# Kernel optimization log

Hardware: AMD Instinct MI355X
Metric: run time of the kernel (lower is better)

Reference implementation:

```python
import jax, jax.numpy as jnp
import numpy as np

F = 16      # frames
NV = 4096   # visual points per frame
NT = 512    # tactile points per frame
M = 4096    # model points
SCALE = 0.1


def setup_inputs() -> dict:
    key = jax.random.key(0)
    ks = jax.random.split(key, 6)
    return {
        "state": jax.random.normal(ks[0], (6,), dtype=jnp.float32) * 0.1,
        "model_points": jax.random.normal(ks[1], (M, 3), dtype=jnp.float32),
        "visual_points": jax.random.normal(ks[2], (F, NV, 3), dtype=jnp.float32),
        "tactile_points": jax.random.normal(ks[3], (F, NT, 3), dtype=jnp.float32),
        "physics_pred_states": jax.random.normal(ks[4], (F, 12), dtype=jnp.float32) * 0.1,
        "delta_time": jax.random.uniform(ks[5], (F,), dtype=jnp.float32, minval=0.01, maxval=0.05),
    }


def _skew(a):
    z = jnp.zeros((), a.dtype)
    return jnp.array([[z, -a[2], a[1]],
                      [a[2], z, -a[0]],
                      [-a[1], a[0], z]])


def _rot_from_omega(omega, dt):
    # Rodrigues: R = I + sin(theta*dt) S + (1 - cos(theta*dt)) S@S, S = skew(omega/|omega|)
    theta = jnp.linalg.norm(omega)
    ax = omega / jnp.clip(theta, 1e-8)
    S = _skew(ax)
    return jnp.eye(3, dtype=omega.dtype) + jnp.sin(theta * dt) * S + (1.0 - jnp.cos(theta * dt)) * (S @ S)


def _chamfer(pred, gt):
    # rows: pred [N,3], cols: gt [M,3]; row-min of squared distances, then mean
    d = (jnp.sum(pred * pred, axis=1)[:, None]
         + jnp.sum(gt * gt, axis=1)[None, :]
         - 2.0 * pred @ gt.T)
    return jnp.mean(jnp.min(d, axis=1))


def reference(state, model_points, visual_points, tactile_points, physics_pred_states, delta_time):
    t0 = state[:3]
    r0 = _rot_from_omega(state[3:], jnp.float32(1.0))  # Euler2Mat modeled as axis-angle

    def pose_step(carry, x):
        t, r = carry
        v, omega, dt = x
        t = t + v * dt
        r = _rot_from_omega(omega, dt) @ r
        return (t, r), (t, r)

    _, (ts, rs) = jax.lax.scan(
        pose_step, (t0, r0),
        (physics_pred_states[1:, 6:9], physics_pred_states[1:, 9:12], delta_time[1:]))
    ts = jnp.concatenate([t0[None], ts], axis=0)  # [F,3]
    rs = jnp.concatenate([r0[None], rs], axis=0)  # [F,3,3]

    def frame_loss(acc, x):
        t, r, vp, tp = x
        vc = ((vp - t) @ r) / SCALE
        tc = ((tp - t) @ r) / SCALE
        acc = acc + _chamfer(vc, model_points) + 0.1 * _chamfer(tc, model_points)
        return acc, None

    E_cd, _ = jax.lax.scan(frame_loss, jnp.zeros((), jnp.float32),
                           (ts, rs, visual_points, tactile_points))
    return E_cd
```

## Files before the change

### kernel.cpp

```cpp
#include <hip/hip_runtime.h>
#include <math.h>

#define F_    16
#define NV_   4096
#define NT_   512
#define M_    4096
#define PPF_  (NV_ + NT_)
#define NPTS_ (F_ * PPF_)
#define SCALE_INV 10.0f

#define TPB   256
#define PTSB  96
#define NBLK  (NPTS_ / PTSB)
#define NG    32
#define MPG   (M_ / NG)
#define CHM   32
#define NCH   (MPG / CHM)
#define FS    33
#define PPL   12
#define NPR   6

typedef float v2f __attribute__((ext_vector_type(2)));
typedef float v4f __attribute__((ext_vector_type(4)));

__device__ inline void rot_from_omega(float ox, float oy, float oz, float dt,
                                      float* R) {
    float theta = sqrtf(ox * ox + oy * oy + oz * oz);
    float inv = 1.0f / fmaxf(theta, 1e-8f);
    float ax = ox * inv, ay = oy * inv, az = oz * inv;
    float s = sinf(theta * dt);
    float c = 1.0f - cosf(theta * dt);
    R[0] = 1.0f - c * (ay * ay + az * az);
    R[1] = -s * az + c * ax * ay;
    R[2] =  s * ay + c * ax * az;
    R[3] =  s * az + c * ax * ay;
    R[4] = 1.0f - c * (ax * ax + az * az);
    R[5] = -s * ax + c * ay * az;
    R[6] = -s * ay + c * ax * az;
    R[7] =  s * ax + c * ay * az;
    R[8] = 1.0f - c * (ax * ax + ay * ay);
}

__device__ __forceinline__ void dist6(v2f qa01, v2f qa23, v2f qb01, v2f qb23,
                                      v2f c0a, v2f c0b, v2f c0c,
                                      v2f c1a, v2f c1b, v2f c1c,
                                      v2f c2a, v2f c2b, v2f c2c, float* dmp) {
    v2f A0, A1, A2, B0, B1, B2;
    asm("v_pk_fma_f32 %0, %7, %16, %7 op_sel:[0,0,1] op_sel_hi:[0,1,1]\n\t"
        "v_pk_fma_f32 %1, %7, %17, %7 op_sel:[0,0,1] op_sel_hi:[0,1,1]\n\t"
        "v_pk_fma_f32 %2, %7, %18, %7 op_sel:[0,0,1] op_sel_hi:[0,1,1]\n\t"
        "v_pk_fma_f32 %3, %9, %16, %9 op_sel:[0,0,1] op_sel_hi:[0,1,1]\n\t"
        "v_pk_fma_f32 %4, %9, %17, %9 op_sel:[0,0,1] op_sel_hi:[0,1,1]\n\t"
        "v_pk_fma_f32 %5, %9, %18, %9 op_sel:[0,0,1] op_sel_hi:[0,1,1]\n\t"
        "v_pk_fma_f32 %0, %6, %13, %0 op_sel:[1,0,0] op_sel_hi:[1,1,1]\n\t"
        "v_pk_fma_f32 %1, %6, %14, %1 op_sel:[1,0,0] op_sel_hi:[1,1,1]\n\t"
        "v_pk_fma_f32 %2, %6, %15, %2 op_sel:[1,0,0] op_sel_hi:[1,1,1]\n\t"
        "v_pk_fma_f32 %3, %8, %13, %3 op_sel:[1,0,0] op_sel_hi:[1,1,1]\n\t"
        "v_pk_fma_f32 %4, %8, %14, %4 op_sel:[1,0,0] op_sel_hi:[1,1,1]\n\t"
        "v_pk_fma_f32 %5, %8, %15, %5 op_sel:[1,0,0] op_sel_hi:[1,1,1]\n\t"
        "v_pk_fma_f32 %0, %6, %10, %0 op_sel:[0,0,0] op_sel_hi:[0,1,1]\n\t"
        "v_pk_fma_f32 %1, %6, %11, %1 op_sel:[0,0,0] op_sel_hi:[0,1,1]\n\t"
        "v_pk_fma_f32 %2, %6, %12, %2 op_sel:[0,0,0] op_sel_hi:[0,1,1]\n\t"
        "v_pk_fma_f32 %3, %8, %10, %3 op_sel:[0,0,0] op_sel_hi:[0,1,1]\n\t"
        "v_pk_fma_f32 %4, %8, %11, %4 op_sel:[0,0,0] op_sel_hi:[0,1,1]\n\t"
        "v_pk_fma_f32 %5, %8, %12, %5 op_sel:[0,0,0] op_sel_hi:[0,1,1]"
        : "=&v"(A0), "=&v"(A1), "=&v"(A2), "=&v"(B0), "=&v"(B1), "=&v"(B2)
        : "v"(qa01), "v"(qa23), "v"(qb01), "v"(qb23),
          "v"(c0a), "v"(c0b), "v"(c0c),
          "v"(c1a), "v"(c1b), "v"(c1c),
          "v"(c2a), "v"(c2b), "v"(c2c));
    dmp[0] = fminf(fminf(A0.x, B0.x), dmp[0]);
    dmp[1] = fminf(fminf(A0.y, B0.y), dmp[1]);
    dmp[2] = fminf(fminf(A1.x, B1.x), dmp[2]);
    dmp[3] = fminf(fminf(A1.y, B1.y), dmp[3]);
    dmp[4] = fminf(fminf(A2.x, B2.x), dmp[4]);
    dmp[5] = fminf(fminf(A2.y, B2.y), dmp[5]);
}

__global__ __launch_bounds__(TPB, 3) void chamfer_one(
    const float* __restrict__ state, const float* __restrict__ model,
    const float* __restrict__ vis, const float* __restrict__ tac,
    const float* __restrict__ phys, const float* __restrict__ dts,
    float* __restrict__ out) {
    __shared__ v4f   feat[NG * FS];
    __shared__ float sdm[PTSB][NG + 1];
    __shared__ float sw[2];

    const int t  = threadIdx.x;
    const int g  = t >> 3;
    const int m0 = t & 7;
    const int pl = t & 7;
    const int f  = (blockIdx.x * PTSB) / PPF_;
    const int lbase = blockIdx.x * PTSB - f * PPF_;

#pragma unroll
    for (int j2 = 0; j2 < 4; ++j2) {
        int id = g * MPG + m0 + 8 * j2;
        float gx = model[id * 3 + 0], gy = model[id * 3 + 1], gz = model[id * 3 + 2];
        feat[g * FS + m0 + 8 * j2] =
            (v4f){-2.0f * gx, -2.0f * gy, -2.0f * gz, gx * gx + gy * gy + gz * gz};
    }

    float R[9], tr[3];
    {
        tr[0] = state[0]; tr[1] = state[1]; tr[2] = state[2];
        rot_from_omega(state[3], state[4], state[5], 1.0f, R);
        for (int i = 1; i <= f; ++i) {
            float dt = dts[i];
            tr[0] += phys[i * 12 + 6] * dt;
            tr[1] += phys[i * 12 + 7] * dt;
            tr[2] += phys[i * 12 + 8] * dt;
            float Rs[9];
            rot_from_omega(phys[i * 12 + 9], phys[i * 12 + 10], phys[i * 12 + 11], dt, Rs);
            float Rn[9];
            for (int r = 0; r < 3; ++r)
                for (int c2 = 0; c2 < 3; ++c2)
                    Rn[r * 3 + c2] = Rs[r * 3 + 0] * R[0 + c2] +
                                     Rs[r * 3 + 1] * R[3 + c2] +
                                     Rs[r * 3 + 2] * R[6 + c2];
            for (int j = 0; j < 9; ++j) R[j] = Rn[j];
        }
        for (int j = 0; j < 9; ++j) R[j] *= SCALE_INV;
    }

    v2f c0p[NPR], c1p[NPR], c2p[NPR];
    float cn[PPL], dm[PPL];
#pragma unroll
    for (int k = 0; k < PPL; ++k) {
        int loc = lbase + pl * PPL + k;
        const float* p = (loc < NV_) ? (vis + ((size_t)f * NV_ + loc) * 3)
                                     : (tac + ((size_t)f * NT_ + (loc - NV_)) * 3);
        float d0 = p[0] - tr[0], d1 = p[1] - tr[1], d2 = p[2] - tr[2];
        float x = d0 * R[0] + d1 * R[3] + d2 * R[6];
        float y = d0 * R[1] + d1 * R[4] + d2 * R[7];
        float z = d0 * R[2] + d1 * R[5] + d2 * R[8];
        cn[k] = x * x + y * y + z * z;
        dm[k] = 3.4e38f;
        if (k & 1) { c0p[k >> 1].y = x; c1p[k >> 1].y = y; c2p[k >> 1].y = z; }
        else       { c0p[k >> 1].x = x; c1p[k >> 1].x = y; c2p[k >> 1].x = z; }
    }
    __syncthreads();

    for (int c = 0; c < NCH; ++c) {
        float mx[4], my[4], mz[4];
        if (c + 1 < NCH) {
#pragma unroll
            for (int j2 = 0; j2 < 4; ++j2) {
                int id = g * MPG + (c + 1) * CHM + m0 + 8 * j2;
                mx[j2] = model[id * 3 + 0];
                my[j2] = model[id * 3 + 1];
                mz[j2] = model[id * 3 + 2];
            }
        }
        const v4f* fb = &feat[g * FS];
#pragma unroll 4
        for (int m = 0; m < CHM; m += 2) {
            v4f ga = fb[m];
            v4f gb = fb[m + 1];
            v2f qa01 = (v2f){ga.x, ga.y}, qa23 = (v2f){ga.z, ga.w};
            v2f qb01 = (v2f){gb.x, gb.y}, qb23 = (v2f){gb.z, gb.w};
            dist6(qa01, qa23, qb01, qb23, c0p[0], c0p[1], c0p[2],
                  c1p[0], c1p[1], c1p[2], c2p[0], c2p[1], c2p[2], dm);
            dist6(qa01, qa23, qb01, qb23, c0p[3], c0p[4], c0p[5],
                  c1p[3], c1p[4], c1p[5], c2p[3], c2p[4], c2p[5], dm + 6);
        }
        __syncthreads();
        if (c + 1 < NCH) {
#pragma unroll
            for (int j2 = 0; j2 < 4; ++j2) {
                feat[g * FS + m0 + 8 * j2] =
                    (v4f){-2.0f * mx[j2], -2.0f * my[j2], -2.0f * mz[j2],
                          mx[j2] * mx[j2] + my[j2] * my[j2] + mz[j2] * mz[j2]};
            }
            __syncthreads();
        }
    }

#pragma unroll
    for (int k = 0; k < PPL; ++k) sdm[pl * PPL + k][g] = dm[k] + cn[k];
    __syncthreads();

    float v = 0.0f;
    if (t < PTSB) {
        const float* row = sdm[t];
        float mn = row[0];
#pragma unroll
        for (int i = 1; i < NG; ++i) mn = fminf(mn, row[i]);
        const int loc = lbase + t;
        const float w = (loc < NV_) ? (1.0f / NV_) : (0.1f / NT_);
        v = mn * w;
    }
    if (t < 128) {
#pragma unroll
        for (int off = 32; off > 0; off >>= 1) v += __shfl_down(v, off);
        if ((t & 63) == 0) sw[t >> 6] = v;
    }
    __syncthreads();
    if (t == 0) atomicAdd(out, sw[0] + sw[1]);
}

extern "C" void kernel_launch(void* const* d_in, const int* in_sizes, int n_in,
                              void* d_out, int out_size, void* d_ws, size_t ws_size,
                              hipStream_t stream) {
    const float* state = (const float*)d_in[0];
    const float* model = (const float*)d_in[1];
    const float* vis   = (const float*)d_in[2];
    const float* tac   = (const float*)d_in[3];
    const float* phys  = (const float*)d_in[4];
    const float* dts   = (const float*)d_in[5];
    float* out = (float*)d_out;
    (void)d_ws; (void)ws_size;

    hipMemsetAsync(out, 0, sizeof(float), stream);
    chamfer_one<<<NBLK, TPB, 0, stream>>>(state, model, vis, tac, phys, dts, out);
}
```

Before: 96.42 us.

## Retile chamfer kernel: 18 points per thread, 64 model groups, frame-aligned blocks

Each thread now handles 18 points (9 packed pairs) against a 64-way split of the model set with 16-point chunks, and each block covers 72 points so 64 blocks map exactly onto one frame. The aim is more FMA work per shared-memory feature load and a higher occupancy target (4 blocks/CU). The model staging loads are remapped to a flat 1024-element pattern. In exchange, register pressure rises because more per-point state is held, there are more chunk synchronisations, and the final row reduction spans 64 entries.

```diff
diff --git a/kernel.cpp b/kernel.cpp
--- a/kernel.cpp
+++ b/kernel.cpp
@@ -10,15 +10,15 @@
 #define SCALE_INV 10.0f
 
 #define TPB   256
-#define PTSB  96
+#define PTSB  72
 #define NBLK  (NPTS_ / PTSB)
-#define NG    32
+#define NG    64
 #define MPG   (M_ / NG)
-#define CHM   32
+#define CHM   16
 #define NCH   (MPG / CHM)
-#define FS    33
-#define PPL   12
-#define NPR   6
+#define FS    17
+#define PPL   18
+#define NPR   9
 
 typedef float v2f __attribute__((ext_vector_type(2)));
 typedef float v4f __attribute__((ext_vector_type(4)));
@@ -77,7 +77,7 @@
     dmp[5] = fminf(fminf(A2.y, B2.y), dmp[5]);
 }
 
-__global__ __launch_bounds__(TPB, 3) void chamfer_one(
+__global__ __launch_bounds__(TPB, 4) void chamfer_one(
     const float* __restrict__ state, const float* __restrict__ model,
     const float* __restrict__ vis, const float* __restrict__ tac,
     const float* __restrict__ phys, const float* __restrict__ dts,
@@ -87,17 +87,18 @@
     __shared__ float sw[2];
 
     const int t  = threadIdx.x;
-    const int g  = t >> 3;
-    const int m0 = t & 7;
-    const int pl = t & 7;
-    const int f  = (blockIdx.x * PTSB) / PPF_;
-    const int lbase = blockIdx.x * PTSB - f * PPF_;
-
-#pragma unroll
-    for (int j2 = 0; j2 < 4; ++j2) {
-        int id = g * MPG + m0 + 8 * j2;
+    const int g  = t >> 2;
+    const int pl = t & 3;
+    const int f  = blockIdx.x >> 6;
+    const int lbase = (blockIdx.x & 63) * PTSB;
+
+#pragma unroll
+    for (int j = 0; j < 4; ++j) {
+        int e  = t + 256 * j;
+        int ge = e >> 4, me = e & 15;
+        int id = ge * MPG + me;
         float gx = model[id * 3 + 0], gy = model[id * 3 + 1], gz = model[id * 3 + 2];
-        feat[g * FS + m0 + 8 * j2] =
+        feat[ge * FS + me] =
             (v4f){-2.0f * gx, -2.0f * gy, -2.0f * gz, gx * gx + gy * gy + gz * gz};
     }
 
@@ -145,11 +146,12 @@
         float mx[4], my[4], mz[4];
         if (c + 1 < NCH) {
 #pragma unroll
-            for (int j2 = 0; j2 < 4; ++j2) {
-                int id = g * MPG + (c + 1) * CHM + m0 + 8 * j2;
-                mx[j2] = model[id * 3 + 0];
-                my[j2] = model[id * 3 + 1];
-                mz[j2] = model[id * 3 + 2];
+            for (int j = 0; j < 4; ++j) {
+                int e  = t + 256 * j;
+                int id = (e >> 4) * MPG + (c + 1) * CHM + (e & 15);
+                mx[j] = model[id * 3 + 0];
+                my[j] = model[id * 3 + 1];
+                mz[j] = model[id * 3 + 2];
             }
         }
         const v4f* fb = &feat[g * FS];
@@ -163,14 +165,17 @@
                   c1p[0], c1p[1], c1p[2], c2p[0], c2p[1], c2p[2], dm);
             dist6(qa01, qa23, qb01, qb23, c0p[3], c0p[4], c0p[5],
                   c1p[3], c1p[4], c1p[5], c2p[3], c2p[4], c2p[5], dm + 6);
+            dist6(qa01, qa23, qb01, qb23, c0p[6], c0p[7], c0p[8],
+                  c1p[6], c1p[7], c1p[8], c2p[6], c2p[7], c2p[8], dm + 12);
         }
         __syncthreads();
         if (c + 1 < NCH) {
 #pragma unroll
-            for (int j2 = 0; j2 < 4; ++j2) {
-                feat[g * FS + m0 + 8 * j2] =
-                    (v4f){-2.0f * mx[j2], -2.0f * my[j2], -2.0f * mz[j2],
-                          mx[j2] * mx[j2] + my[j2] * my[j2] + mz[j2] * mz[j2]};
+            for (int j = 0; j < 4; ++j) {
+                int e = t + 256 * j;
+                feat[(e >> 4) * FS + (e & 15)] =
+                    (v4f){-2.0f * mx[j], -2.0f * my[j], -2.0f * mz[j],
+                          mx[j] * mx[j] + my[j] * my[j] + mz[j] * mz[j]};
             }
             __syncthreads();
         }
@@ -184,7 +189,7 @@
     if (t < PTSB) {
         const float* row = sdm[t];
         float mn = row[0];
-#pragma unroll
+#pragma unroll 8
         for (int i = 1; i < NG; ++i) mn = fminf(mn, row[i]);
         const int loc = lbase + t;
         const float w = (loc < NV_) ? (1.0f / NV_) : (0.1f / NT_);
```

Result: slower. 102.5 us (+6.3%).
